# Performance work log

Hardware: AMD Instinct MI355X
Metric: run time of the kernel (lower is better)

## Reference

```python
import jax, jax.numpy as jnp
import numpy as np

N = 50000
E = 800000
IN_CH = 512
HID = 64
H1 = 4
NUM_CLASSES = 16
NEG_SLOPE = 0.2


def _add_self_loops(edge_index, n):
    loop = jnp.arange(n, dtype=edge_index.dtype)
    src = jnp.concatenate([edge_index[0], loop])
    dst = jnp.concatenate([edge_index[1], loop])
    return src, dst


def gat_conv(x, edge_index, W, att_src, att_dst, bias, heads, out_ch, concat):
    n = x.shape[0]
    src, dst = _add_self_loops(edge_index, n)
    # linear projection -> [N, H, C]
    h = (x @ W).reshape(n, heads, out_ch)
    # per-node attention logits [N, H]
    a_src = jnp.einsum('nhc,hc->nh', h, att_src)
    a_dst = jnp.einsum('nhc,hc->nh', h, att_dst)
    # per-edge logits, leaky relu
    e = a_src[src] + a_dst[dst]                       # [E', H]
    e = jnp.where(e >= 0, e, NEG_SLOPE * e)
    # segment softmax over edges grouped by destination node
    emax = jax.ops.segment_max(e, dst, num_segments=n)  # [N, H]
    ex = jnp.exp(e - emax[dst])
    denom = jax.ops.segment_sum(ex, dst, num_segments=n)
    alpha = ex / denom[dst]                            # [E', H]
    # message = gathered source features weighted by alpha, scatter-add to dst
    msg = h[src] * alpha[..., None]                    # [E', H, C]
    out = jax.ops.segment_sum(msg, dst, num_segments=n)  # [N, H, C]
    if concat:
        out = out.reshape(n, heads * out_ch)
    else:
        out = out.mean(axis=1)
    return out + bias


def setup_inputs() -> dict:
    key = jax.random.key(0)
    ks = jax.random.split(key, 12)
    x = jax.random.normal(ks[0], (N, IN_CH), dtype=jnp.float32)
    edge_index = jax.random.randint(ks[1], (2, E), 0, N, dtype=jnp.int64)
    s1 = 1.0 / np.sqrt(IN_CH)
    W1 = jax.random.normal(ks[2], (IN_CH, H1 * HID), dtype=jnp.float32) * s1
    att_src1 = jax.random.normal(ks[3], (H1, HID), dtype=jnp.float32) * (1.0 / np.sqrt(HID))
    att_dst1 = jax.random.normal(ks[4], (H1, HID), dtype=jnp.float32) * (1.0 / np.sqrt(HID))
    b1 = jnp.zeros((H1 * HID,), dtype=jnp.float32)
    s2 = 1.0 / np.sqrt(H1 * HID)
    W2 = jax.random.normal(ks[5], (H1 * HID, NUM_CLASSES), dtype=jnp.float32) * s2
    att_src2 = jax.random.normal(ks[6], (1, NUM_CLASSES), dtype=jnp.float32) * (1.0 / np.sqrt(NUM_CLASSES))
    att_dst2 = jax.random.normal(ks[7], (1, NUM_CLASSES), dtype=jnp.float32) * (1.0 / np.sqrt(NUM_CLASSES))
    b2 = jnp.zeros((NUM_CLASSES,), dtype=jnp.float32)
    return {
        'x': x, 'edge_index': edge_index,
        'W1': W1, 'att_src1': att_src1, 'att_dst1': att_dst1, 'b1': b1,
        'W2': W2, 'att_src2': att_src2, 'att_dst2': att_dst2, 'b2': b2,
    }


def reference(x, edge_index, W1, att_src1, att_dst1, b1, W2, att_src2, att_dst2, b2):
    # eval mode: dropout (drop_rate) is inactive
    h = gat_conv(x, edge_index, W1, att_src1, att_dst1, b1, H1, HID, concat=True)
    h = jax.nn.elu(h)
    out = gat_conv(h, edge_index, W2, att_src2, att_dst2, b2, 1, NUM_CLASSES, concat=False)
    return out
```

## Files before the change

### kernel.cpp

```cpp
#include <hip/hip_runtime.h>
#include <hip/hip_bf16.h>
#include <math.h>

#define NN 50000
#define EE 800000
#define INCH 512
#define C1 256
#define NC 16
#define NEG 0.2f

typedef __attribute__((ext_vector_type(8))) short bf16x8;
typedef __attribute__((ext_vector_type(4))) float f32x4;

__device__ inline short f2bf(float f) {
    __hip_bfloat16 h = __float2bfloat16(f);
    return *reinterpret_cast<short*>(&h);
}

__device__ inline void unpack4(uint2 rv, float& v0, float& v1, float& v2, float& v3) {
    v0 = __uint_as_float(rv.x << 16);
    v1 = __uint_as_float(rv.x & 0xFFFF0000u);
    v2 = __uint_as_float(rv.y << 16);
    v3 = __uint_as_float(rv.y & 0xFFFF0000u);
}

__global__ __launch_bounds__(256) void k_w1t(const float* __restrict__ W1,
                                             __hip_bfloat16* __restrict__ W1t) {
    __shared__ float t[32][33];
    int k0 = blockIdx.x * 32, n0 = blockIdx.y * 32;
    int tx = threadIdx.x & 31, ty = threadIdx.x >> 5;
#pragma unroll
    for (int i = 0; i < 4; i++) {
        t[ty + i * 8][tx] = W1[(size_t)(k0 + ty + i * 8) * C1 + n0 + tx];
    }
    __syncthreads();
#pragma unroll
    for (int i = 0; i < 4; i++) {
        W1t[(size_t)(n0 + ty + i * 8) * INCH + k0 + tx] = __float2bfloat16(t[tx][ty + i * 8]);
    }
}

#define BM3 64
#define BK3 64
#define NBM 782
#define GEMM1_BLKS 3136
#define HIST_BLKS 3125
__global__ __launch_bounds__(256) void k_gemm1(const float* __restrict__ x,
                                               const __hip_bfloat16* __restrict__ W1t,
                                               const float* __restrict__ as1,
                                               const float* __restrict__ ad1,
                                               unsigned short* __restrict__ h1b,
                                               float* __restrict__ a_src,
                                               float* __restrict__ a_dst,
                                               const int* __restrict__ edst,
                                               int* __restrict__ cnt) {
    int l = blockIdx.x;
    if (l >= GEMM1_BLKS) {
        int e = (l - GEMM1_BLKS) * 256 + threadIdx.x;
        if (e < EE) atomicAdd(&cnt[edst[e]], 1);
        return;
    }
    int g = l >> 5, r = l & 31;
    int head = r >> 3, slot = r & 7;
    int bmi = g * 8 + slot;
    if (bmi >= NBM) return;
    int bm = bmi * BM3;
    int bn = head * 64;

    __shared__ __align__(16) short Ah[BM3 * BK3];
    __shared__ __align__(16) short Bl[BM3 * BK3];
    int tid = threadIdx.x;
    int wm = tid >> 6, lane = tid & 63;
    int quad = lane >> 4, l16 = lane & 15;

    f32x4 acc[4];
#pragma unroll
    for (int j = 0; j < 4; j++) acc[j] = (f32x4){0.f, 0.f, 0.f, 0.f};

    for (int kt = 0; kt < INCH; kt += BK3) {
#pragma unroll
        for (int i = 0; i < 4; i++) {
            int idx = tid + 256 * i;
            int row = idx >> 4, c4 = idx & 15;
            int m = bm + row; if (m >= NN) m = NN - 1;
            float4 v = *(const float4*)&x[(size_t)m * INCH + kt + c4 * 4];
            short4 h4 = make_short4(f2bf(v.x), f2bf(v.y), f2bf(v.z), f2bf(v.w));
            int swc = (c4 >> 1) ^ (row & 7);
            *(short4*)&Ah[row * BK3 + swc * 8 + (c4 & 1) * 4] = h4;
        }
#pragma unroll
        for (int i = 0; i < 2; i++) {
            int idx = tid + 256 * i;
            int row = idx >> 3, c8 = idx & 7;
            float4 v = *(const float4*)(W1t + (size_t)(bn + row) * INCH + kt + c8 * 8);
            int swc = c8 ^ (row & 7);
            *(float4*)&Bl[row * BK3 + swc * 8] = v;
        }
        __syncthreads();
#pragma unroll
        for (int ks = 0; ks < 2; ks++) {
            int lc = (ks * 4 + quad);
            bf16x8 af, bfr[4];
            {
                int row = wm * 16 + l16;
                af = *(bf16x8*)&Ah[row * BK3 + (lc ^ (l16 & 7)) * 8];
            }
#pragma unroll
            for (int ni = 0; ni < 4; ni++) {
                int row = ni * 16 + l16;
                bfr[ni] = *(bf16x8*)&Bl[row * BK3 + (lc ^ (l16 & 7)) * 8];
            }
#pragma unroll
            for (int ni = 0; ni < 4; ni++)
                acc[ni] = __builtin_amdgcn_mfma_f32_16x16x32_bf16(af, bfr[ni], acc[ni], 0, 0, 0);
        }
        __syncthreads();
    }
#pragma unroll
    for (int r2 = 0; r2 < 4; r2++) {
        int gm = bm + wm * 16 + quad * 4 + r2;
        if (gm < NN) {
#pragma unroll
            for (int ni = 0; ni < 4; ni++)
                h1b[(size_t)gm * C1 + bn + ni * 16 + l16] = (unsigned short)f2bf(acc[ni][r2]);
        }
    }
    float aw[4], dw[4];
#pragma unroll
    for (int ni = 0; ni < 4; ni++) {
        aw[ni] = as1[bn + ni * 16 + l16];
        dw[ni] = ad1[bn + ni * 16 + l16];
    }
#pragma unroll
    for (int r2 = 0; r2 < 4; r2++) {
        float ps = acc[0][r2] * aw[0] + acc[1][r2] * aw[1] + acc[2][r2] * aw[2] + acc[3][r2] * aw[3];
        float pd = acc[0][r2] * dw[0] + acc[1][r2] * dw[1] + acc[2][r2] * dw[2] + acc[3][r2] * dw[3];
#pragma unroll
        for (int off = 8; off; off >>= 1) {
            ps += __shfl_xor(ps, off, 16);
            pd += __shfl_xor(pd, off, 16);
        }
        if (l16 == 0) {
            int gm = bm + wm * 16 + quad * 4 + r2;
            if (gm < NN) {
                a_src[gm * 4 + head] = ps;
                a_dst[gm * 4 + head] = pd;
            }
        }
    }
}

__global__ __launch_bounds__(256) void k_scan1(const int* __restrict__ cnt, int* __restrict__ partial) {
    __shared__ int s[256];
    int i = blockIdx.x * 256 + threadIdx.x;
    s[threadIdx.x] = (i < NN) ? cnt[i] : 0;
    __syncthreads();
    for (int off = 128; off; off >>= 1) {
        if (threadIdx.x < off) s[threadIdx.x] += s[threadIdx.x + off];
        __syncthreads();
    }
    if (threadIdx.x == 0) partial[blockIdx.x] = s[0];
}

__global__ __launch_bounds__(256) void k_scan2(int* partial, int nb) {
    __shared__ int s[256];
    int t = threadIdx.x;
    int v = (t < nb) ? partial[t] : 0;
    s[t] = v;
    __syncthreads();
    for (int off = 1; off < 256; off <<= 1) {
        int y = (t >= off) ? s[t - off] : 0;
        __syncthreads();
        s[t] += y;
        __syncthreads();
    }
    if (t < nb) partial[t] = s[t] - v;
}

__global__ __launch_bounds__(256) void k_scan3(const int* __restrict__ cnt, const int* __restrict__ partial,
                                               int* __restrict__ row_off, int* __restrict__ cursor) {
    __shared__ int s[256];
    int t = threadIdx.x;
    int i = blockIdx.x * 256 + t;
    int v = (i < NN) ? cnt[i] : 0;
    s[t] = v;
    __syncthreads();
    for (int off = 1; off < 256; off <<= 1) {
        int y = (t >= off) ? s[t - off] : 0;
        __syncthreads();
        s[t] += y;
        __syncthreads();
    }
    if (i < NN) {
        int o = partial[blockIdx.x] + s[t] - v;
        row_off[i] = o;
        cursor[i] = o;
    }
}

__global__ __launch_bounds__(256) void k_place(const int* __restrict__ esrc, const int* __restrict__ edst,
                                               int* __restrict__ cursor, int* __restrict__ csr) {
    int e = blockIdx.x * 256 + threadIdx.x;
    if (e >= EE) return;
    int d = edst[e];
    int s = esrc[e];
    int pos = atomicAdd(&cursor[d], 1);
    csr[pos] = s;
}

__global__ __launch_bounds__(256) void k_agg1(const unsigned short* __restrict__ h1b,
                                              const int* __restrict__ csr,
                                              const int* __restrict__ row_off, const int* __restrict__ cnt,
                                              const float* __restrict__ a_src, const float* __restrict__ a_dst,
                                              const float* __restrict__ b1, float* __restrict__ h2in) {
    int tid = threadIdx.x;
    int wv = tid >> 6, lane = tid & 63;
    int n = blockIdx.x * 4 + wv;
    if (n >= NN) return;
    int head = lane >> 4;
    const uint2* rows = (const uint2*)h1b;

    float adn = a_dst[n * 4 + head];
    float es = a_src[n * 4 + head] + adn;
    es = fmaxf(es, NEG * es);
    float wse = __expf(es);
    float denom = wse;
    float a0, a1, a2, a3;
    {
        uint2 rv = rows[(size_t)n * 64 + lane];
        float v0, v1, v2, v3;
        unpack4(rv, v0, v1, v2, v3);
        a0 = wse * v0; a1 = wse * v1; a2 = wse * v2; a3 = wse * v3;
    }

    int base = row_off[n], deg = cnt[n];
    for (int c0 = 0; c0 < deg; c0 += 64) {
        int sv = 0;
        if (c0 + lane < deg) sv = csr[base + c0 + lane];
        int m = deg - c0; if (m > 64) m = 64;
        int k = 0;
        for (; k + 4 <= m; k += 4) {
            int s0 = __shfl(sv, k + 0), s1 = __shfl(sv, k + 1);
            int s2 = __shfl(sv, k + 2), s3 = __shfl(sv, k + 3);
            float e0 = a_src[s0 * 4 + head] + adn;
            float e1 = a_src[s1 * 4 + head] + adn;
            float e2 = a_src[s2 * 4 + head] + adn;
            float e3 = a_src[s3 * 4 + head] + adn;
            uint2 r0 = rows[(size_t)s0 * 64 + lane];
            uint2 r1 = rows[(size_t)s1 * 64 + lane];
            uint2 r2 = rows[(size_t)s2 * 64 + lane];
            uint2 r3 = rows[(size_t)s3 * 64 + lane];
            e0 = fmaxf(e0, NEG * e0); e1 = fmaxf(e1, NEG * e1);
            e2 = fmaxf(e2, NEG * e2); e3 = fmaxf(e3, NEG * e3);
            float w0 = __expf(e0), w1 = __expf(e1), w2 = __expf(e2), w3 = __expf(e3);
            float v0, v1, v2, v3;
            unpack4(r0, v0, v1, v2, v3);
            denom += w0; a0 += w0 * v0; a1 += w0 * v1; a2 += w0 * v2; a3 += w0 * v3;
            unpack4(r1, v0, v1, v2, v3);
            denom += w1; a0 += w1 * v0; a1 += w1 * v1; a2 += w1 * v2; a3 += w1 * v3;
            unpack4(r2, v0, v1, v2, v3);
            denom += w2; a0 += w2 * v0; a1 += w2 * v1; a2 += w2 * v2; a3 += w2 * v3;
            unpack4(r3, v0, v1, v2, v3);
            denom += w3; a0 += w3 * v0; a1 += w3 * v1; a2 += w3 * v2; a3 += w3 * v3;
        }
        for (; k < m; k++) {
            int s0 = __shfl(sv, k);
            float e0 = a_src[s0 * 4 + head] + adn;
            uint2 r0 = rows[(size_t)s0 * 64 + lane];
            e0 = fmaxf(e0, NEG * e0);
            float w0 = __expf(e0);
            float v0, v1, v2, v3;
            unpack4(r0, v0, v1, v2, v3);
            denom += w0; a0 += w0 * v0; a1 += w0 * v1; a2 += w0 * v2; a3 += w0 * v3;
        }
    }
    float inv = 1.f / denom;
    float4 bv = *(const float4*)&b1[lane * 4];
    float o0 = a0 * inv + bv.x, o1 = a1 * inv + bv.y;
    float o2 = a2 * inv + bv.z, o3 = a3 * inv + bv.w;
    o0 = o0 > 0.f ? o0 : expm1f(o0);
    o1 = o1 > 0.f ? o1 : expm1f(o1);
    o2 = o2 > 0.f ? o2 : expm1f(o2);
    o3 = o3 > 0.f ? o3 : expm1f(o3);
    *(float4*)&h2in[(size_t)n * C1 + lane * 4] = make_float4(o0, o1, o2, o3);
}

#define LDB 260
__global__ __launch_bounds__(256) void k_gemm2(const float* __restrict__ h2in,
                                               const float* __restrict__ W2,
                                               const float* __restrict__ as2, const float* __restrict__ ad2,
                                               float* __restrict__ h2,
                                               float* __restrict__ a_src2, float* __restrict__ a_dst2) {
    __shared__ __align__(16) float ws_t[16 * LDB];
    __shared__ __align__(16) float hs[16 * LDB];
    int tid = threadIdx.x;
#pragma unroll
    for (int i = 0; i < 16; i++) {
        int idx = i * 256 + tid;
        int k = idx >> 4, col = idx & 15;
        ws_t[col * LDB + k] = W2[idx];
    }
    int nb = blockIdx.x * 16;
    for (int i = 0; i < 16; i++) {
        int n = nb + i;
        hs[i * LDB + tid] = (n < NN) ? h2in[(size_t)n * C1 + tid] : 0.f;
    }
    __syncthreads();
    int r = tid >> 4, col = tid & 15;
    float acc = 0.f;
    for (int k = 0; k < 256; k += 4) {
        float4 hv = *(const float4*)&hs[r * LDB + k];
        float4 wv = *(const float4*)&ws_t[col * LDB + k];
        acc += hv.x * wv.x + hv.y * wv.y + hv.z * wv.z + hv.w * wv.w;
    }
    float pa = acc * as2[col], pb = acc * ad2[col];
#pragma unroll
    for (int off = 8; off; off >>= 1) {
        pa += __shfl_xor(pa, off, 16);
        pb += __shfl_xor(pb, off, 16);
    }
    int n = nb + r;
    if (n < NN) {
        h2[(size_t)n * NC + col] = acc;
        if (col == 0) { a_src2[n] = pa; a_dst2[n] = pb; }
    }
}

__global__ __launch_bounds__(256) void k_agg2(const float* __restrict__ h2,
                                              const int* __restrict__ csr,
                                              const int* __restrict__ row_off, const int* __restrict__ cnt,
                                              const float* __restrict__ a_src2, const float* __restrict__ a_dst2,
                                              const float* __restrict__ b2, float* __restrict__ out) {
    int tid = threadIdx.x;
    int r = tid >> 4, col = tid & 15;
    int n = blockIdx.x * 16 + r;
    if (n >= NN) return;
    float adn = a_dst2[n];
    float es = a_src2[n] + adn;
    es = fmaxf(es, NEG * es);
    float wse = __expf(es);
    float denom = wse;
    float acc = wse * h2[(size_t)n * NC + col];
    int base = row_off[n], deg = cnt[n];
    int k = 0;
    for (; k + 4 <= deg; k += 4) {
        int s0 = csr[base + k + 0], s1 = csr[base + k + 1];
        int s2 = csr[base + k + 2], s3 = csr[base + k + 3];
        float e0 = a_src2[s0] + adn, e1 = a_src2[s1] + adn;
        float e2 = a_src2[s2] + adn, e3 = a_src2[s3] + adn;
        float v0 = h2[(size_t)s0 * NC + col], v1 = h2[(size_t)s1 * NC + col];
        float v2 = h2[(size_t)s2 * NC + col], v3 = h2[(size_t)s3 * NC + col];
        e0 = fmaxf(e0, NEG * e0); e1 = fmaxf(e1, NEG * e1);
        e2 = fmaxf(e2, NEG * e2); e3 = fmaxf(e3, NEG * e3);
        float w0 = __expf(e0), w1 = __expf(e1), w2 = __expf(e2), w3 = __expf(e3);
        denom += w0; acc += w0 * v0;
        denom += w1; acc += w1 * v1;
        denom += w2; acc += w2 * v2;
        denom += w3; acc += w3 * v3;
    }
    for (; k < deg; k++) {
        int s0 = csr[base + k];
        float e0 = a_src2[s0] + adn;
        e0 = fmaxf(e0, NEG * e0);
        float w0 = __expf(e0);
        denom += w0;
        acc += w0 * h2[(size_t)s0 * NC + col];
    }
    out[(size_t)n * NC + col] = acc / denom + b2[col];
}

extern "C" void kernel_launch(void* const* d_in, const int* in_sizes, int n_in,
                              void* d_out, int out_size, void* d_ws, size_t ws_size,
                              hipStream_t stream) {
    const float* x   = (const float*)d_in[0];
    const int*   ei  = (const int*)d_in[1];
    const int*   esrc = ei;
    const int*   edst = ei + EE;
    const float* W1  = (const float*)d_in[2];
    const float* as1 = (const float*)d_in[3];
    const float* ad1 = (const float*)d_in[4];
    const float* b1  = (const float*)d_in[5];
    const float* W2  = (const float*)d_in[6];
    const float* as2 = (const float*)d_in[7];
    const float* ad2 = (const float*)d_in[8];
    const float* b2  = (const float*)d_in[9];
    float* out = (float*)d_out;

    char* w = (char*)d_ws;
    size_t off = 0;
    auto alloc = [&](size_t bytes) -> void* {
        void* p = w + off;
        off += (bytes + 255) & ~(size_t)255;
        return p;
    };
    unsigned short* h1b = (unsigned short*)alloc((size_t)NN * C1 * 2);
    float* h2in   = (float*)alloc((size_t)NN * C1 * 4);
    int*   csr    = (int*)alloc((size_t)EE * 4);
    float* h2     = (float*)alloc((size_t)NN * NC * 4);
    float* a_src1 = (float*)alloc((size_t)NN * 4 * 4);
    float* a_dst1 = (float*)alloc((size_t)NN * 4 * 4);
    int*   cnt    = (int*)alloc((size_t)NN * 4);
    int*   row_off= (int*)alloc((size_t)NN * 4);
    int*   cursor = (int*)alloc((size_t)NN * 4);
    float* a_src2 = (float*)alloc((size_t)NN * 4);
    float* a_dst2 = (float*)alloc((size_t)NN * 4);
    int*   partial= (int*)alloc(256 * 4);
    __hip_bfloat16* W1t = (__hip_bfloat16*)alloc((size_t)C1 * INCH * 2);

    hipMemsetAsync(cnt, 0, (size_t)NN * 4, stream);

    const int NBLK = (NN + 255) / 256;

    k_w1t<<<dim3(INCH / 32, C1 / 32), 256, 0, stream>>>(W1, W1t);
    k_gemm1<<<GEMM1_BLKS + HIST_BLKS, 256, 0, stream>>>(x, W1t, as1, ad1, h1b,
                                                        a_src1, a_dst1, edst, cnt);
    k_scan1<<<NBLK, 256, 0, stream>>>(cnt, partial);
    k_scan2<<<1, 256, 0, stream>>>(partial, NBLK);
    k_scan3<<<NBLK, 256, 0, stream>>>(cnt, partial, row_off, cursor);
    k_place<<<HIST_BLKS, 256, 0, stream>>>(esrc, edst, cursor, csr);
    k_agg1<<<(NN + 3) / 4, 256, 0, stream>>>(h1b, csr, row_off, cnt, a_src1, a_dst1, b1, h2in);
    k_gemm2<<<(NN + 15) / 16, 256, 0, stream>>>(h2in, W2, as2, ad2, h2, a_src2, a_dst2);
    k_agg2<<<(NN + 15) / 16, 256, 0, stream>>>(h2, csr, row_off, cnt, a_src2, a_dst2, b2, out);
}
```

Before: 382.5 us.

## Fuse second-layer projection and attention logits into first aggregation epilogue

The layer-2 linear projection and its attention logit computation move into the end of the layer-1 aggregation kernel. Each wave multiplies its node's ELU output by W2 and reduces across lanes with shuffles. This removes the full-size intermediate h2in buffer write and re-read and drops one kernel launch. In exchange, each wave does a 64-lane butterfly reduction of 16 values, and the extra registers may lower occupancy of the gather-bound aggregation kernel.

Measured after the change: 421.6 us. 1.1x slower.

```diff
diff --git a/kernel.cpp b/kernel.cpp
--- a/kernel.cpp
+++ b/kernel.cpp
@@ -212,7 +212,11 @@
                                               const int* __restrict__ csr,
                                               const int* __restrict__ row_off, const int* __restrict__ cnt,
                                               const float* __restrict__ a_src, const float* __restrict__ a_dst,
-                                              const float* __restrict__ b1, float* __restrict__ h2in) {
+                                              const float* __restrict__ b1,
+                                              const float* __restrict__ W2,
+                                              const float* __restrict__ as2, const float* __restrict__ ad2,
+                                              float* __restrict__ h2,
+                                              float* __restrict__ a_src2, float* __restrict__ a_dst2) {
     int tid = threadIdx.x;
     int wv = tid >> 6, lane = tid & 63;
     int n = blockIdx.x * 4 + wv;
@@ -276,53 +280,44 @@
     }
     float inv = 1.f / denom;
     float4 bv = *(const float4*)&b1[lane * 4];
-    float o0 = a0 * inv + bv.x, o1 = a1 * inv + bv.y;
-    float o2 = a2 * inv + bv.z, o3 = a3 * inv + bv.w;
-    o0 = o0 > 0.f ? o0 : expm1f(o0);
-    o1 = o1 > 0.f ? o1 : expm1f(o1);
-    o2 = o2 > 0.f ? o2 : expm1f(o2);
-    o3 = o3 > 0.f ? o3 : expm1f(o3);
-    *(float4*)&h2in[(size_t)n * C1 + lane * 4] = make_float4(o0, o1, o2, o3);
-}
-
-#define LDB 260
-__global__ __launch_bounds__(256) void k_gemm2(const float* __restrict__ h2in,
-                                               const float* __restrict__ W2,
-                                               const float* __restrict__ as2, const float* __restrict__ ad2,
-                                               float* __restrict__ h2,
-                                               float* __restrict__ a_src2, float* __restrict__ a_dst2) {
-    __shared__ __align__(16) float ws_t[16 * LDB];
-    __shared__ __align__(16) float hs[16 * LDB];
-    int tid = threadIdx.x;
-#pragma unroll
-    for (int i = 0; i < 16; i++) {
-        int idx = i * 256 + tid;
-        int k = idx >> 4, col = idx & 15;
-        ws_t[col * LDB + k] = W2[idx];
-    }
-    int nb = blockIdx.x * 16;
-    for (int i = 0; i < 16; i++) {
-        int n = nb + i;
-        hs[i * LDB + tid] = (n < NN) ? h2in[(size_t)n * C1 + tid] : 0.f;
-    }
-    __syncthreads();
-    int r = tid >> 4, col = tid & 15;
-    float acc = 0.f;
-    for (int k = 0; k < 256; k += 4) {
-        float4 hv = *(const float4*)&hs[r * LDB + k];
-        float4 wv = *(const float4*)&ws_t[col * LDB + k];
-        acc += hv.x * wv.x + hv.y * wv.y + hv.z * wv.z + hv.w * wv.w;
-    }
-    float pa = acc * as2[col], pb = acc * ad2[col];
-#pragma unroll
-    for (int off = 8; off; off >>= 1) {
-        pa += __shfl_xor(pa, off, 16);
-        pb += __shfl_xor(pb, off, 16);
-    }
-    int n = nb + r;
-    if (n < NN) {
-        h2[(size_t)n * NC + col] = acc;
-        if (col == 0) { a_src2[n] = pa; a_dst2[n] = pb; }
+    float o[4];
+    o[0] = a0 * inv + bv.x; o[1] = a1 * inv + bv.y;
+    o[2] = a2 * inv + bv.z; o[3] = a3 * inv + bv.w;
+#pragma unroll
+    for (int j = 0; j < 4; j++) o[j] = o[j] > 0.f ? o[j] : expm1f(o[j]);
+
+    float p[16];
+#pragma unroll
+    for (int c2 = 0; c2 < 16; c2++) p[c2] = 0.f;
+#pragma unroll
+    for (int j = 0; j < 4; j++) {
+        const float4* wr = (const float4*)&W2[(size_t)(lane * 4 + j) * NC];
+        float4 w0 = wr[0], w1 = wr[1], w2v = wr[2], w3 = wr[3];
+        float oj = o[j];
+        p[0] += oj * w0.x;  p[1] += oj * w0.y;  p[2] += oj * w0.z;  p[3] += oj * w0.w;
+        p[4] += oj * w1.x;  p[5] += oj * w1.y;  p[6] += oj * w1.z;  p[7] += oj * w1.w;
+        p[8] += oj * w2v.x; p[9] += oj * w2v.y; p[10] += oj * w2v.z; p[11] += oj * w2v.w;
+        p[12] += oj * w3.x; p[13] += oj * w3.y; p[14] += oj * w3.z; p[15] += oj * w3.w;
+    }
+#pragma unroll
+    for (int off = 1; off < 64; off <<= 1) {
+#pragma unroll
+        for (int c2 = 0; c2 < 16; c2++) p[c2] += __shfl_xor(p[c2], off, 64);
+    }
+    if (lane == 0) {
+        float* hrow = &h2[(size_t)n * NC];
+        *(float4*)&hrow[0]  = make_float4(p[0], p[1], p[2], p[3]);
+        *(float4*)&hrow[4]  = make_float4(p[4], p[5], p[6], p[7]);
+        *(float4*)&hrow[8]  = make_float4(p[8], p[9], p[10], p[11]);
+        *(float4*)&hrow[12] = make_float4(p[12], p[13], p[14], p[15]);
+        float pa = 0.f, pb = 0.f;
+#pragma unroll
+        for (int c2 = 0; c2 < 16; c2++) {
+            pa += p[c2] * as2[c2];
+            pb += p[c2] * ad2[c2];
+        }
+        a_src2[n] = pa;
+        a_dst2[n] = pb;
     }
 }
 
@@ -394,7 +389,6 @@
         return p;
     };
     unsigned short* h1b = (unsigned short*)alloc((size_t)NN * C1 * 2);
-    float* h2in   = (float*)alloc((size_t)NN * C1 * 4);
     int*   csr    = (int*)alloc((size_t)EE * 4);
     float* h2     = (float*)alloc((size_t)NN * NC * 4);
     float* a_src1 = (float*)alloc((size_t)NN * 4 * 4);
@@ -418,7 +412,7 @@
     k_scan2<<<1, 256, 0, stream>>>(partial, NBLK);
     k_scan3<<<NBLK, 256, 0, stream>>>(cnt, partial, row_off, cursor);
     k_place<<<HIST_BLKS, 256, 0, stream>>>(esrc, edst, cursor, csr);
-    k_agg1<<<(NN + 3) / 4, 256, 0, stream>>>(h1b, csr, row_off, cnt, a_src1, a_dst1, b1, h2in);
-    k_gemm2<<<(NN + 15) / 16, 256, 0, stream>>>(h2in, W2, as2, ad2, h2, a_src2, a_dst2);
+    k_agg1<<<(NN + 3) / 4, 256, 0, stream>>>(h1b, csr, row_off, cnt, a_src1, a_dst1, b1,
+                                             W2, as2, ad2, h2, a_src2, a_dst2);
     k_agg2<<<(NN + 15) / 16, 256, 0, stream>>>(h2, csr, row_off, cnt, a_src2, a_dst2, b2, out);
 }
```

## Store layer-1 output in bf16 and compute layer-2 projection with MFMA

Applied to the files above, without the earlier changes.

The aggregation kernel now writes its ELU output as bf16 instead of fp32, which halves that intermediate buffer. The second GEMM is rewritten to use bf16 16x16x32 MFMA instructions, reading rows directly without LDS staging. W2 is transposed and converted to bf16 inside the existing single-block scan kernel. This cuts memory traffic for the 50000x256 intermediate and the GEMM2 FLOP cost, at the cost of bf16 rounding in the second layer's input.

Measured after the change: 360.0 us. 5.9% less time.

```diff
diff --git a/kernel.cpp b/kernel.cpp
--- a/kernel.cpp
+++ b/kernel.cpp
@@ -162,9 +162,15 @@
     if (threadIdx.x == 0) partial[blockIdx.x] = s[0];
 }
 
-__global__ __launch_bounds__(256) void k_scan2(int* partial, int nb) {
+__global__ __launch_bounds__(256) void k_scan2(int* partial, int nb,
+                                               const float* __restrict__ W2,
+                                               __hip_bfloat16* __restrict__ w2t) {
     __shared__ int s[256];
     int t = threadIdx.x;
+#pragma unroll
+    for (int c = 0; c < NC; c++) {
+        w2t[(size_t)c * C1 + t] = __float2bfloat16(W2[(size_t)t * NC + c]);
+    }
     int v = (t < nb) ? partial[t] : 0;
     s[t] = v;
     __syncthreads();
@@ -212,7 +218,8 @@
                                               const int* __restrict__ csr,
                                               const int* __restrict__ row_off, const int* __restrict__ cnt,
                                               const float* __restrict__ a_src, const float* __restrict__ a_dst,
-                                              const float* __restrict__ b1, float* __restrict__ h2in) {
+                                              const float* __restrict__ b1,
+                                              unsigned short* __restrict__ h2inb) {
     int tid = threadIdx.x;
     int wv = tid >> 6, lane = tid & 63;
     int n = blockIdx.x * 4 + wv;
@@ -282,47 +289,46 @@
     o1 = o1 > 0.f ? o1 : expm1f(o1);
     o2 = o2 > 0.f ? o2 : expm1f(o2);
     o3 = o3 > 0.f ? o3 : expm1f(o3);
-    *(float4*)&h2in[(size_t)n * C1 + lane * 4] = make_float4(o0, o1, o2, o3);
-}
-
-#define LDB 260
-__global__ __launch_bounds__(256) void k_gemm2(const float* __restrict__ h2in,
-                                               const float* __restrict__ W2,
+    uint2 pk;
+    pk.x = (unsigned int)(unsigned short)f2bf(o0) | ((unsigned int)(unsigned short)f2bf(o1) << 16);
+    pk.y = (unsigned int)(unsigned short)f2bf(o2) | ((unsigned int)(unsigned short)f2bf(o3) << 16);
+    *(uint2*)&h2inb[(size_t)n * C1 + lane * 4] = pk;
+}
+
+__global__ __launch_bounds__(256) void k_gemm2(const unsigned short* __restrict__ h2inb,
+                                               const __hip_bfloat16* __restrict__ w2t,
                                                const float* __restrict__ as2, const float* __restrict__ ad2,
                                                float* __restrict__ h2,
                                                float* __restrict__ a_src2, float* __restrict__ a_dst2) {
-    __shared__ __align__(16) float ws_t[16 * LDB];
-    __shared__ __align__(16) float hs[16 * LDB];
     int tid = threadIdx.x;
-#pragma unroll
-    for (int i = 0; i < 16; i++) {
-        int idx = i * 256 + tid;
-        int k = idx >> 4, col = idx & 15;
-        ws_t[col * LDB + k] = W2[idx];
-    }
-    int nb = blockIdx.x * 16;
-    for (int i = 0; i < 16; i++) {
-        int n = nb + i;
-        hs[i * LDB + tid] = (n < NN) ? h2in[(size_t)n * C1 + tid] : 0.f;
-    }
-    __syncthreads();
-    int r = tid >> 4, col = tid & 15;
-    float acc = 0.f;
-    for (int k = 0; k < 256; k += 4) {
-        float4 hv = *(const float4*)&hs[r * LDB + k];
-        float4 wv = *(const float4*)&ws_t[col * LDB + k];
-        acc += hv.x * wv.x + hv.y * wv.y + hv.z * wv.z + hv.w * wv.w;
-    }
-    float pa = acc * as2[col], pb = acc * ad2[col];
-#pragma unroll
-    for (int off = 8; off; off >>= 1) {
-        pa += __shfl_xor(pa, off, 16);
-        pb += __shfl_xor(pb, off, 16);
-    }
-    int n = nb + r;
-    if (n < NN) {
-        h2[(size_t)n * NC + col] = acc;
-        if (col == 0) { a_src2[n] = pa; a_dst2[n] = pb; }
+    int wave = tid >> 6, lane = tid & 63;
+    int quad = lane >> 4, l16 = lane & 15;
+    int mbase = blockIdx.x * 64 + wave * 16;
+    if (mbase >= NN) return;
+    int mrow = mbase + l16; if (mrow >= NN) mrow = NN - 1;
+    const bf16x8* arow = (const bf16x8*)(h2inb + (size_t)mrow * C1);
+    f32x4 acc = (f32x4){0.f, 0.f, 0.f, 0.f};
+#pragma unroll
+    for (int ks = 0; ks < 8; ks++) {
+        bf16x8 af = arow[ks * 4 + quad];
+        bf16x8 bfv = *(const bf16x8*)(w2t + (size_t)l16 * C1 + ks * 32 + quad * 8);
+        acc = __builtin_amdgcn_mfma_f32_16x16x32_bf16(af, bfv, acc, 0, 0, 0);
+    }
+    float a2 = as2[l16], d2 = ad2[l16];
+#pragma unroll
+    for (int r = 0; r < 4; r++) {
+        int gm = mbase + quad * 4 + r;
+        if (gm < NN) h2[(size_t)gm * NC + l16] = acc[r];
+        float pa = acc[r] * a2, pb = acc[r] * d2;
+#pragma unroll
+        for (int off = 8; off; off >>= 1) {
+            pa += __shfl_xor(pa, off, 16);
+            pb += __shfl_xor(pb, off, 16);
+        }
+        if (l16 == 0 && gm < NN) {
+            a_src2[gm] = pa;
+            a_dst2[gm] = pb;
+        }
     }
 }
 
@@ -393,8 +399,8 @@
         off += (bytes + 255) & ~(size_t)255;
         return p;
     };
-    unsigned short* h1b = (unsigned short*)alloc((size_t)NN * C1 * 2);
-    float* h2in   = (float*)alloc((size_t)NN * C1 * 4);
+    unsigned short* h1b   = (unsigned short*)alloc((size_t)NN * C1 * 2);
+    unsigned short* h2inb = (unsigned short*)alloc((size_t)NN * C1 * 2);
     int*   csr    = (int*)alloc((size_t)EE * 4);
     float* h2     = (float*)alloc((size_t)NN * NC * 4);
     float* a_src1 = (float*)alloc((size_t)NN * 4 * 4);
@@ -406,6 +412,7 @@
     float* a_dst2 = (float*)alloc((size_t)NN * 4);
     int*   partial= (int*)alloc(256 * 4);
     __hip_bfloat16* W1t = (__hip_bfloat16*)alloc((size_t)C1 * INCH * 2);
+    __hip_bfloat16* w2t = (__hip_bfloat16*)alloc((size_t)NC * C1 * 2);
 
     hipMemsetAsync(cnt, 0, (size_t)NN * 4, stream);
 
@@ -415,10 +422,10 @@
     k_gemm1<<<GEMM1_BLKS + HIST_BLKS, 256, 0, stream>>>(x, W1t, as1, ad1, h1b,
                                                         a_src1, a_dst1, edst, cnt);
     k_scan1<<<NBLK, 256, 0, stream>>>(cnt, partial);
-    k_scan2<<<1, 256, 0, stream>>>(partial, NBLK);
+    k_scan2<<<1, 256, 0, stream>>>(partial, NBLK, W2, w2t);
     k_scan3<<<NBLK, 256, 0, stream>>>(cnt, partial, row_off, cursor);
     k_place<<<HIST_BLKS, 256, 0, stream>>>(esrc, edst, cursor, csr);
-    k_agg1<<<(NN + 3) / 4, 256, 0, stream>>>(h1b, csr, row_off, cnt, a_src1, a_dst1, b1, h2in);
-    k_gemm2<<<(NN + 15) / 16, 256, 0, stream>>>(h2in, W2, as2, ad2, h2, a_src2, a_dst2);
+    k_agg1<<<(NN + 3) / 4, 256, 0, stream>>>(h1b, csr, row_off, cnt, a_src1, a_dst1, b1, h2inb);
+    k_gemm2<<<(NN + 63) / 64, 256, 0, stream>>>(h2inb, w2t, as2, ad2, h2, a_src2, a_dst2);
     k_agg2<<<(NN + 15) / 16, 256, 0, stream>>>(h2, csr, row_off, cnt, a_src2, a_dst2, b2, out);
 }
```
